# Kernel tuning notes

Hardware: AMD Instinct MI355X
Metric: run time of the kernel (lower is better)

Reference implementation:

```python
import jax, jax.numpy as jnp
import numpy as np
from jax import lax

D = 1024; L = 2; NS = 16; PD = 64; B_ = 64; K_ = 128; H_ = 32; W_ = 32


def setup_inputs():
    ks = jax.random.split(jax.random.key(0), 16)
    def rn(i, shape, s=0.02):
        return jax.random.normal(ks[i], shape, dtype=jnp.float32) * s
    return {
        "slots": jax.random.normal(ks[0], (B_, K_, D), dtype=jnp.float32),
        "keep_mask": jnp.ones((B_, K_), jnp.float32),
        "attn_maps": jax.random.uniform(ks[1], (B_, K_, H_ * W_), dtype=jnp.float32),
        "H": H_, "W": W_,
        "pos_W1": rn(2, (4 * PD, D)), "pos_b1": jnp.zeros((D,), jnp.float32),
        "pos_W2": rn(3, (D, D)), "pos_b2": jnp.zeros((D,), jnp.float32),
        "ssm_W_in": rn(4, (2, L, D, D)), "ssm_b_in": jnp.zeros((2, L, D), jnp.float32),
        "ssm_W_dt": rn(5, (2, L, D, D)), "ssm_b_dt": jnp.zeros((2, L, D), jnp.float32),
        "ssm_W_B": rn(6, (2, L, D, NS)), "ssm_W_C": rn(7, (2, L, D, NS)),
        "ssm_A_log": rn(8, (2, L, D, NS), 1.0), "ssm_D": rn(9, (2, L, D), 1.0),
        "ssm_W_out": rn(10, (2, L, D, D)), "ssm_b_out": jnp.zeros((2, L, D), jnp.float32),
        "merge_W": rn(11, (L, 2 * D, D)), "merge_b": jnp.zeros((L, D), jnp.float32),
        "norm_g": jnp.ones((L, D), jnp.float32), "norm_b": jnp.zeros((L, D), jnp.float32),
        "ffn_lng": jnp.ones((L, D), jnp.float32), "ffn_lnb": jnp.zeros((L, D), jnp.float32),
        "ffn_W1": rn(12, (L, D, 4 * D)), "ffn_b1": jnp.zeros((L, 4 * D), jnp.float32),
        "ffn_W2": rn(13, (L, 4 * D, D)), "ffn_b2": jnp.zeros((L, D), jnp.float32),
    }


def _ln(x, g, b):
    m = jnp.mean(x, -1, keepdims=True)
    v = jnp.mean((x - m) ** 2, -1, keepdims=True)
    return (x - m) * lax.rsqrt(v + 1e-5) * g + b


def _gelu(x):
    return jax.nn.gelu(x, approximate=False)


def _hilbert_order(centroids):
    # vectorized xy2d Hilbert index on a 16x16 grid, then argsort per batch
    gs = 16
    cx = jnp.clip(centroids[..., 0] * (gs - 1), 0, gs - 1).astype(jnp.int32)
    cy = jnp.clip(centroids[..., 1] * (gs - 1), 0, gs - 1).astype(jnp.int32)
    x, y = cx, cy
    d = jnp.zeros_like(cx)
    s = gs // 2
    while s > 0:
        rx = ((x & s) > 0).astype(jnp.int32)
        ry = ((y & s) > 0).astype(jnp.int32)
        d = d + s * s * ((3 * rx) ^ ry)
        x1 = jnp.where(rx == 1, s - 1 - x, x)
        y1 = jnp.where(rx == 1, s - 1 - y, y)
        xn = jnp.where(ry == 0, y1, x)
        yn = jnp.where(ry == 0, x1, y)
        x, y = xn, yn
        s //= 2
    return jnp.argsort(d, axis=-1)


def _ssm(x, W_in, b_in, W_dt, b_dt, W_B, W_C, A_log, D_skip, W_out, b_out):
    # Mamba-style diagonal selective scan: h_t = exp(dt*A)h_{t-1} + dt*B_t*u_t; y_t = C_t.h_t + D*u_t
    u = x @ W_in + b_in                    # [B,K,D]
    dt = jax.nn.softplus(x @ W_dt + b_dt)  # [B,K,D]
    Bc = x @ W_B                           # [B,K,NS]
    Cc = x @ W_C                           # [B,K,NS]
    A = -jnp.exp(A_log)                    # [D,NS]

    def step(h, inp):
        u_t, dt_t, B_t, C_t = inp
        h = jnp.exp(dt_t[..., None] * A) * h + dt_t[..., None] * B_t[:, None, :] * u_t[..., None]
        y = jnp.einsum('bdn,bn->bd', h, C_t) + D_skip * u_t
        return h, y

    h0 = jnp.zeros((x.shape[0], x.shape[-1], A.shape[-1]), x.dtype)
    xs = (u.swapaxes(0, 1), dt.swapaxes(0, 1), Bc.swapaxes(0, 1), Cc.swapaxes(0, 1))
    _, ys = lax.scan(step, h0, xs)
    return ys.swapaxes(0, 1) @ W_out + b_out


def _forward(slots, keep_mask, attn_maps, H, W, pos_W1, pos_b1, pos_W2, pos_b2,
             ssm_W_in, ssm_b_in, ssm_W_dt, ssm_b_dt, ssm_W_B, ssm_W_C, ssm_A_log,
             ssm_D, ssm_W_out, ssm_b_out, merge_W, merge_b, norm_g, norm_b,
             ffn_lng, ffn_lnb, ffn_W1, ffn_b1, ffn_W2, ffn_b2):
    B, K, Dm = slots.shape
    # slot centroids from attention maps
    attn = attn_maps[:, :K, :]
    gy = jnp.arange(H, dtype=slots.dtype) / max(H - 1, 1)
    gx = jnp.arange(W, dtype=slots.dtype) / max(W - 1, 1)
    grid_y, grid_x = jnp.meshgrid(gy, gx, indexing='ij')
    coords = jnp.stack([grid_x.ravel(), grid_y.ravel()], -1)  # [N,2]
    attn_prob = attn / (jnp.sum(attn, -1, keepdims=True) + 1e-8)
    centroids = jnp.einsum('bkn,nc->bkc', attn_prob, coords)  # [B,K,2]
    # sinusoidal spatial encoding of (centroid, spread)
    feats = jnp.concatenate([centroids, jnp.full_like(centroids, 0.1)], -1)  # [B,K,4]
    freqs = 1.0 / 10000.0 ** (jnp.arange(0, PD, 2, dtype=slots.dtype) / PD)
    ang = feats[..., None] * freqs * 3.14159                   # [B,K,4,PD/2]
    enc = jnp.concatenate([jnp.sin(ang), jnp.cos(ang)], -1).reshape(B, K, 4 * PD)
    pos_enc = _gelu(enc @ pos_W1 + pos_b1) @ pos_W2 + pos_b2
    slots = slots + pos_enc
    order = _hilbert_order(centroids)         # [B,K] (same every layer)
    reverse = jnp.argsort(order, -1)
    for i in range(merge_W.shape[0]):
        residual = slots
        ordered = jnp.take_along_axis(slots, order[..., None], 1)
        f = _ssm(ordered, ssm_W_in[0, i], ssm_b_in[0, i], ssm_W_dt[0, i], ssm_b_dt[0, i],
                 ssm_W_B[0, i], ssm_W_C[0, i], ssm_A_log[0, i], ssm_D[0, i],
                 ssm_W_out[0, i], ssm_b_out[0, i])
        bwd = jnp.flip(_ssm(jnp.flip(ordered, 1), ssm_W_in[1, i], ssm_b_in[1, i],
                            ssm_W_dt[1, i], ssm_b_dt[1, i], ssm_W_B[1, i], ssm_W_C[1, i],
                            ssm_A_log[1, i], ssm_D[1, i], ssm_W_out[1, i], ssm_b_out[1, i]), 1)
        merged = jnp.concatenate([f, bwd], -1) @ merge_W[i] + merge_b[i]
        unord = jnp.take_along_axis(merged, reverse[..., None], 1)
        slots = _ln(residual + unord, norm_g[i], norm_b[i])
        h = _ln(slots, ffn_lng[i], ffn_lnb[i])
        slots = slots + (_gelu(h @ ffn_W1[i] + ffn_b1[i]) @ ffn_W2[i] + ffn_b2[i])
        slots = slots * keep_mask[..., None]
    return slots, centroids


def reference(slots, keep_mask, attn_maps, H, W, pos_W1, pos_b1, pos_W2, pos_b2,
              ssm_W_in, ssm_b_in, ssm_W_dt, ssm_b_dt, ssm_W_B, ssm_W_C, ssm_A_log,
              ssm_D, ssm_W_out, ssm_b_out, merge_W, merge_b, norm_g, norm_b,
              ffn_lng, ffn_lnb, ffn_W1, ffn_b1, ffn_W2, ffn_b2):
    return _forward(slots, keep_mask, attn_maps, H, W, pos_W1, pos_b1, pos_W2, pos_b2,
                    ssm_W_in, ssm_b_in, ssm_W_dt, ssm_b_dt, ssm_W_B, ssm_W_C, ssm_A_log,
                    ssm_D, ssm_W_out, ssm_b_out, merge_W, merge_b, norm_g, norm_b,
                    ffn_lng, ffn_lnb, ffn_W1, ffn_b1, ffn_W2, ffn_b2)
```

## Files before the change

### kernel.cpp

```cpp
#include <hip/hip_runtime.h>
#include <hip/hip_bf16.h>
#include <math.h>

typedef __attribute__((ext_vector_type(8))) short short8;
typedef __attribute__((ext_vector_type(4))) float f32x4;
typedef __hip_bfloat16 bf16;

#define GAS(p) ((const __attribute__((address_space(1))) void*)(p))
#define LAS(p) ((__attribute__((address_space(3))) void*)(p))

__device__ __forceinline__ float gelu_exact(float x) {
    return 0.5f * x * (1.0f + erff(x * 0.70710678118654752f));
}
__device__ __forceinline__ float softplus_f(float x) {
    return (x > 20.f) ? x : log1pf(__expf(x));
}

__global__ void transpose_to_bf16(const float* __restrict__ in, bf16* __restrict__ out,
                                  int R, int C) {
    __shared__ float tile[32][33];
    int c0 = blockIdx.x * 32, r0 = blockIdx.y * 32;
    for (int i = threadIdx.y; i < 32; i += 8) {
        int r = r0 + i, c = c0 + threadIdx.x;
        tile[i][threadIdx.x] = (r < R && c < C) ? in[(size_t)r * C + c] : 0.f;
    }
    __syncthreads();
    for (int i = threadIdx.y; i < 32; i += 8) {
        int c = c0 + i, r = r0 + threadIdx.x;
        if (c < C && r < R) out[(size_t)c * R + r] = __float2bfloat16(tile[threadIdx.x][i]);
    }
}

__global__ void centroid_kernel(const float* __restrict__ attn, float* __restrict__ out_cent,
                                int* __restrict__ hd) {
    int row = blockIdx.x * 4 + (threadIdx.x >> 6);
    int lane = threadIdx.x & 63;
    const float* ap = attn + (size_t)row * 1024;
    float s = 0.f, sx = 0.f, sy = 0.f;
    for (int i = lane; i < 1024; i += 64) {
        float a = ap[i];
        float cxn = (float)(i & 31) * (1.0f / 31.0f);
        float cyn = (float)(i >> 5) * (1.0f / 31.0f);
        s += a; sx += a * cxn; sy += a * cyn;
    }
#pragma unroll
    for (int o = 32; o; o >>= 1) {
        s += __shfl_xor(s, o); sx += __shfl_xor(sx, o); sy += __shfl_xor(sy, o);
    }
    if (lane == 0) {
        float inv = 1.0f / (s + 1e-8f);
        float cx = sx * inv, cy = sy * inv;
        out_cent[row * 2] = cx;
        out_cent[row * 2 + 1] = cy;
        int x = (int)fminf(fmaxf(cx * 15.f, 0.f), 15.f);
        int y = (int)fminf(fmaxf(cy * 15.f, 0.f), 15.f);
        int d = 0;
        for (int s2 = 8; s2 > 0; s2 >>= 1) {
            int rx = (x & s2) ? 1 : 0, ry = (y & s2) ? 1 : 0;
            d += s2 * s2 * ((3 * rx) ^ ry);
            int x1 = rx ? (s2 - 1 - x) : x;
            int y1 = rx ? (s2 - 1 - y) : y;
            int xn = (ry == 0) ? y1 : x;
            int yn = (ry == 0) ? x1 : y;
            x = xn; y = yn;
        }
        hd[row] = d;
    }
}

__global__ void order_kernel(const int* __restrict__ hd, int* __restrict__ order) {
    __shared__ int dsh[128];
    int b = blockIdx.x, tid = threadIdx.x;
    dsh[tid] = hd[b * 128 + tid];
    __syncthreads();
    int mine = dsh[tid], rank = 0;
    for (int j = 0; j < 128; ++j) {
        int dj = dsh[j];
        rank += (dj < mine) || (dj == mine && j < tid);
    }
    order[b * 128 + rank] = tid;
}

__global__ void enc_kernel(const float* __restrict__ cent, bf16* __restrict__ enc) {
    int row = blockIdx.x, tid = threadIdx.x;
    int f = tid >> 6, s = tid & 63;
    float feat = (f == 0) ? cent[row * 2] : (f == 1) ? cent[row * 2 + 1] : 0.1f;
    int i = s & 31;
    float freq = powf(10000.f, -(float)i * (1.f / 32.f));
    float ang = feat * freq * 3.14159f;
    float v = (s < 32) ? sinf(ang) : cosf(ang);
    enc[(size_t)row * 256 + tid] = __float2bfloat16(v);
}

template <int EPI>
__launch_bounds__(256)
__global__ void gemm_bt(const bf16* __restrict__ A, int lda,
                        const bf16* __restrict__ Bt, int K, int ldc,
                        float* __restrict__ outF, bf16* __restrict__ outB,
                        const float* __restrict__ bias1, const float* __restrict__ bias2,
                        const float* __restrict__ resid, const float* __restrict__ mask) {
    __shared__ __align__(16) short a_sh[128 * 64];
    __shared__ __align__(16) short b_sh[128 * 64];
    const int tid = threadIdx.x;
    const int lane = tid & 63;
    const int wid = tid >> 6;
    const int wr = wid >> 1, wc = wid & 1;
    const int row0 = blockIdx.y * 128;
    const int col0 = blockIdx.x * 128;

    f32x4 acc[4][4] = {};

    const int nk = K >> 6;
    for (int kt = 0; kt < nk; ++kt) {
        __syncthreads();
#pragma unroll
        for (int c = 0; c < 4; ++c) {
            int slot = c * 256 + tid;
            int r = slot >> 3;
            int ks = (slot & 7) ^ (r & 7);
            const bf16* ga = A + (size_t)(row0 + r) * lda + (kt << 6) + (ks << 3);
            __builtin_amdgcn_global_load_lds(GAS(ga), LAS((char*)a_sh + slot * 16), 16, 0, 0);
            const bf16* gb = Bt + (size_t)(col0 + r) * K + (kt << 6) + (ks << 3);
            __builtin_amdgcn_global_load_lds(GAS(gb), LAS((char*)b_sh + slot * 16), 16, 0, 0);
        }
        __syncthreads();
#pragma unroll
        for (int kk = 0; kk < 2; ++kk) {
            short8 af[4], bfr[4];
            int kb = (kk << 2) + (lane >> 4);
#pragma unroll
            for (int m = 0; m < 4; ++m) {
                int r = wr * 64 + m * 16 + (lane & 15);
                af[m] = *(const short8*)(a_sh + ((r << 3) + (kb ^ (r & 7))) * 8);
            }
#pragma unroll
            for (int n = 0; n < 4; ++n) {
                int r = wc * 64 + n * 16 + (lane & 15);
                bfr[n] = *(const short8*)(b_sh + ((r << 3) + (kb ^ (r & 7))) * 8);
            }
#pragma unroll
            for (int m = 0; m < 4; ++m)
#pragma unroll
                for (int n = 0; n < 4; ++n)
                    acc[m][n] = __builtin_amdgcn_mfma_f32_16x16x32_bf16(af[m], bfr[n], acc[m][n], 0, 0, 0);
        }
    }

#pragma unroll
    for (int m = 0; m < 4; ++m) {
#pragma unroll
        for (int n = 0; n < 4; ++n) {
#pragma unroll
            for (int q = 0; q < 4; ++q) {
                int r = row0 + wr * 64 + m * 16 + ((lane >> 4) << 2) + q;
                int c = col0 + wc * 64 + n * 16 + (lane & 15);
                float v = acc[m][n][q];
                size_t idx = (size_t)r * ldc + c;
                if constexpr (EPI == 0) {
                    v = gelu_exact(v + bias1[c]);
                    outB[idx] = __float2bfloat16(v);
                } else if constexpr (EPI == 1) {
                    v += bias1[c] + resid[idx];
                    outF[idx] = v;
                    outB[idx] = __float2bfloat16(v);
                } else if constexpr (EPI == 2) {
                    if (c < 1024) {
                        outF[idx] = v + bias1[c];
                    } else if (c < 2048) {
                        outF[idx] = softplus_f(v + bias2[c - 1024]);
                    } else if (c < 2080) {
                        outF[idx] = v;
                    }
                } else if constexpr (EPI == 3) {
                    outB[idx] = __float2bfloat16(v + bias1[c]);
                } else if constexpr (EPI == 4) {
                    outF[idx] = v + bias1[c] + resid[(size_t)r * 1024 + c];
                } else {
                    float sv = resid[idx] + v + bias1[c];
                    sv *= mask[r];
                    outF[idx] = sv;
                    outB[idx] = __float2bfloat16(sv);
                }
            }
        }
    }
}

__launch_bounds__(256)
__global__ void scan_kernel(const float* __restrict__ udt, const int* __restrict__ order,
                            const float* __restrict__ A_log, const float* __restrict__ Dsk,
                            bf16* __restrict__ ycat, int layer, int dir) {
    __shared__ float bc_sh[128 * 32];
    __shared__ int ord_sh[128];
    const int tid = threadIdx.x;
    const int dch = blockIdx.x, b = blockIdx.y;
    if (tid < 128) ord_sh[tid] = order[b * 128 + tid];
    __syncthreads();
    for (int i = tid; i < 128 * 32; i += 256) {
        int t = i >> 5, n = i & 31;
        int p = ord_sh[t];
        bc_sh[i] = udt[(size_t)(b * 128 + p) * 2176 + 2048 + n];
    }
    __syncthreads();
    const int d = dch * 256 + tid;
    float a[16], h[16];
    const float* al = A_log + ((size_t)((dir * 2 + layer) * 1024 + d)) * 16;
#pragma unroll
    for (int n = 0; n < 16; ++n) { a[n] = -__expf(al[n]); h[n] = 0.f; }
    const float dsk = Dsk[(dir * 2 + layer) * 1024 + d];

    float uf[4], df[4];
#pragma unroll
    for (int j = 0; j < 4; ++j) {
        int t = dir ? (127 - j) : j;
        size_t rb = (size_t)(b * 128 + ord_sh[t]) * 2176;
        uf[j] = udt[rb + d];
        df[j] = udt[rb + 1024 + d];
    }
    for (int s0 = 0; s0 < 128; s0 += 4) {
#pragma unroll
        for (int j = 0; j < 4; ++j) {
            int s = s0 + j;
            int t = dir ? (127 - s) : s;
            float u = uf[j], dt = df[j];
            int s2 = s + 4;
            if (s2 < 128) {
                int t2 = dir ? (127 - s2) : s2;
                size_t rb2 = (size_t)(b * 128 + ord_sh[t2]) * 2176;
                uf[j] = udt[rb2 + d];
                df[j] = udt[rb2 + 1024 + d];
            }
            float y = dsk * u;
            float dtu = dt * u;
#pragma unroll
            for (int n = 0; n < 16; ++n) {
                h[n] = __expf(dt * a[n]) * h[n] + dtu * bc_sh[t * 32 + n];
                y += h[n] * bc_sh[t * 32 + 16 + n];
            }
            ycat[(size_t)(b * 128 + ord_sh[t]) * 2048 + dir * 1024 + d] = __float2bfloat16(y);
        }
    }
}

__launch_bounds__(256)
__global__ void ln2_kernel(const float* __restrict__ tmp, float* __restrict__ slots,
                           bf16* __restrict__ hout,
                           const float* __restrict__ g1, const float* __restrict__ b1,
                           const float* __restrict__ g2, const float* __restrict__ b2) {
    __shared__ float red[16];
    const int tid = threadIdx.x, row = blockIdx.x;
    const int lane = tid & 63, wid = tid >> 6;
    const float4 x = ((const float4*)(tmp + (size_t)row * 1024))[tid];
    float s = x.x + x.y + x.z + x.w;
    float ss = x.x * x.x + x.y * x.y + x.z * x.z + x.w * x.w;
#pragma unroll
    for (int o = 32; o; o >>= 1) { s += __shfl_xor(s, o); ss += __shfl_xor(ss, o); }
    if (lane == 0) { red[wid] = s; red[4 + wid] = ss; }
    __syncthreads();
    float S = red[0] + red[1] + red[2] + red[3];
    float SS = red[4] + red[5] + red[6] + red[7];
    float m = S * (1.f / 1024.f);
    float inv = rsqrtf(SS * (1.f / 1024.f) - m * m + 1e-5f);
    int c = tid * 4;
    float4 sv;
    sv.x = (x.x - m) * inv * g1[c] + b1[c];
    sv.y = (x.y - m) * inv * g1[c + 1] + b1[c + 1];
    sv.z = (x.z - m) * inv * g1[c + 2] + b1[c + 2];
    sv.w = (x.w - m) * inv * g1[c + 3] + b1[c + 3];
    ((float4*)(slots + (size_t)row * 1024))[tid] = sv;
    float s2 = sv.x + sv.y + sv.z + sv.w;
    float ss2 = sv.x * sv.x + sv.y * sv.y + sv.z * sv.z + sv.w * sv.w;
#pragma unroll
    for (int o = 32; o; o >>= 1) { s2 += __shfl_xor(s2, o); ss2 += __shfl_xor(ss2, o); }
    if (lane == 0) { red[8 + wid] = s2; red[12 + wid] = ss2; }
    __syncthreads();
    float S2 = red[8] + red[9] + red[10] + red[11];
    float SS2 = red[12] + red[13] + red[14] + red[15];
    float m2 = S2 * (1.f / 1024.f);
    float inv2 = rsqrtf(SS2 * (1.f / 1024.f) - m2 * m2 + 1e-5f);
    size_t ob = (size_t)row * 1024 + c;
    hout[ob]     = __float2bfloat16((sv.x - m2) * inv2 * g2[c] + b2[c]);
    hout[ob + 1] = __float2bfloat16((sv.y - m2) * inv2 * g2[c + 1] + b2[c + 1]);
    hout[ob + 2] = __float2bfloat16((sv.z - m2) * inv2 * g2[c + 2] + b2[c + 2]);
    hout[ob + 3] = __float2bfloat16((sv.w - m2) * inv2 * g2[c + 3] + b2[c + 3]);
}

static void launch_gemm(int epi, int N, hipStream_t st, const bf16* A, int lda,
                        const bf16* Bt, int K, int ldc, float* outF, bf16* outB,
                        const float* b1, const float* b2, const float* resid,
                        const float* mask) {
    dim3 grid(N / 128, 64);
    switch (epi) {
        case 0: gemm_bt<0><<<grid, 256, 0, st>>>(A, lda, Bt, K, ldc, outF, outB, b1, b2, resid, mask); break;
        case 1: gemm_bt<1><<<grid, 256, 0, st>>>(A, lda, Bt, K, ldc, outF, outB, b1, b2, resid, mask); break;
        case 2: gemm_bt<2><<<grid, 256, 0, st>>>(A, lda, Bt, K, ldc, outF, outB, b1, b2, resid, mask); break;
        case 3: gemm_bt<3><<<grid, 256, 0, st>>>(A, lda, Bt, K, ldc, outF, outB, b1, b2, resid, mask); break;
        case 4: gemm_bt<4><<<grid, 256, 0, st>>>(A, lda, Bt, K, ldc, outF, outB, b1, b2, resid, mask); break;
        default: gemm_bt<5><<<grid, 256, 0, st>>>(A, lda, Bt, K, ldc, outF, outB, b1, b2, resid, mask); break;
    }
}

static void launch_tr(hipStream_t st, const float* in, bf16* out, int R, int C) {
    dim3 g((C + 31) / 32, (R + 31) / 32);
    transpose_to_bf16<<<g, dim3(32, 8), 0, st>>>(in, out, R, C);
}

extern "C" void kernel_launch(void* const* d_in, const int* in_sizes, int n_in,
                              void* d_out, int out_size, void* d_ws, size_t ws_size,
                              hipStream_t stream) {
    (void)in_sizes; (void)n_in; (void)out_size;
    const float* slots_in = (const float*)d_in[0];
    const float* keep     = (const float*)d_in[1];
    const float* attn     = (const float*)d_in[2];
    const float* pos_W1   = (const float*)d_in[5];
    const float* pos_b1   = (const float*)d_in[6];
    const float* pos_W2   = (const float*)d_in[7];
    const float* pos_b2   = (const float*)d_in[8];
    const float* W_in     = (const float*)d_in[9];
    const float* b_in     = (const float*)d_in[10];
    const float* W_dt     = (const float*)d_in[11];
    const float* b_dt     = (const float*)d_in[12];
    const float* W_B      = (const float*)d_in[13];
    const float* W_C      = (const float*)d_in[14];
    const float* A_log    = (const float*)d_in[15];
    const float* Dsk      = (const float*)d_in[16];
    const float* W_out    = (const float*)d_in[17];
    const float* b_out    = (const float*)d_in[18];
    const float* merge_W  = (const float*)d_in[19];
    const float* merge_b  = (const float*)d_in[20];
    const float* norm_g   = (const float*)d_in[21];
    const float* norm_b   = (const float*)d_in[22];
    const float* ffn_lng  = (const float*)d_in[23];
    const float* ffn_lnb  = (const float*)d_in[24];
    const float* ffn_W1   = (const float*)d_in[25];
    const float* ffn_b1   = (const float*)d_in[26];
    const float* ffn_W2   = (const float*)d_in[27];
    const float* ffn_b2   = (const float*)d_in[28];

    float* out_slots = (float*)d_out;
    float* out_cent  = out_slots + (size_t)8192 * 1024;

    char* ws = (char*)d_ws;
    size_t off = 0;
    auto alloc = [&](size_t bytes) -> char* {
        char* r = ws + off;
        off += (bytes + 255) & ~(size_t)255;
        return r;
    };
    bf16* wpool    = (bf16*)alloc((size_t)4096 * 1024 * 2);
    bf16* slots_bf = (bf16*)alloc((size_t)8192 * 1024 * 2);
    int*  hd       = (int*)alloc((size_t)8192 * 4);
    int*  order    = (int*)alloc((size_t)8192 * 4);
    char* scratch  = alloc((size_t)104857600);
    if (ws_size < off) return;

    float* udt  = (float*)scratch;
    bf16*  ycat = (bf16*)(scratch + 71303168);
    bf16*  encb = (bf16*)scratch;
    bf16*  h1   = (bf16*)(scratch + 4194304);
    bf16*  fbwd = (bf16*)scratch;
    float* tmp  = (float*)(scratch + 33554432);
    bf16*  hbuf = (bf16*)(scratch + 71303168);
    bf16*  mid  = (bf16*)scratch;

    centroid_kernel<<<2048, 256, 0, stream>>>(attn, out_cent, hd);
    order_kernel<<<64, 128, 0, stream>>>(hd, order);
    enc_kernel<<<8192, 256, 0, stream>>>(out_cent, encb);

    bf16* posW1t = wpool;
    bf16* posW2t = wpool + 262144;
    launch_tr(stream, pos_W1, posW1t, 256, 1024);
    launch_tr(stream, pos_W2, posW2t, 1024, 1024);
    launch_gemm(0, 1024, stream, encb, 256, posW1t, 256, 1024, nullptr, h1,
                pos_b1, nullptr, nullptr, nullptr);
    launch_gemm(1, 1024, stream, h1, 1024, posW2t, 1024, 1024, out_slots, slots_bf,
                pos_b2, nullptr, slots_in, nullptr);

    for (int l = 0; l < 2; ++l) {
        for (int dir = 0; dir < 2; ++dir) {
            size_t wsl = (size_t)(dir * 2 + l);
            launch_tr(stream, W_in + wsl * 1048576, wpool, 1024, 1024);
            launch_tr(stream, W_dt + wsl * 1048576, wpool + (size_t)1024 * 1024, 1024, 1024);
            launch_tr(stream, W_B + wsl * 16384, wpool + (size_t)2048 * 1024, 1024, 16);
            launch_tr(stream, W_C + wsl * 16384, wpool + (size_t)2064 * 1024, 1024, 16);
            launch_gemm(2, 2176, stream, slots_bf, 1024, wpool, 1024, 2176, udt, nullptr,
                        b_in + wsl * 1024, b_dt + wsl * 1024, nullptr, nullptr);
            scan_kernel<<<dim3(4, 64), 256, 0, stream>>>(udt, order, A_log, Dsk, ycat, l, dir);
        }
        for (int dir = 0; dir < 2; ++dir) {
            size_t wsl = (size_t)(dir * 2 + l);
            launch_tr(stream, W_out + wsl * 1048576, wpool, 1024, 1024);
            launch_gemm(3, 1024, stream, ycat + dir * 1024, 2048, wpool, 1024, 2048,
                        nullptr, fbwd + dir * 1024, b_out + wsl * 1024, nullptr, nullptr, nullptr);
        }
        launch_tr(stream, merge_W + (size_t)l * 2097152, wpool, 2048, 1024);
        launch_gemm(4, 1024, stream, fbwd, 2048, wpool, 2048, 1024, tmp, nullptr,
                    merge_b + l * 1024, nullptr, out_slots, nullptr);
        ln2_kernel<<<8192, 256, 0, stream>>>(tmp, out_slots, hbuf,
                                             norm_g + l * 1024, norm_b + l * 1024,
                                             ffn_lng + l * 1024, ffn_lnb + l * 1024);
        launch_tr(stream, ffn_W1 + (size_t)l * 4194304, wpool, 1024, 4096);
        launch_gemm(0, 4096, stream, hbuf, 1024, wpool, 1024, 4096, nullptr, mid,
                    ffn_b1 + (size_t)l * 4096, nullptr, nullptr, nullptr);
        launch_tr(stream, ffn_W2 + (size_t)l * 4194304, wpool, 4096, 1024);
        launch_gemm(5, 1024, stream, mid, 4096, wpool, 4096, 1024, out_slots, slots_bf,
                    ffn_b2 + l * 1024, nullptr, out_slots, keep);
    }
}
```

Baseline: 1.919 ms.

## Use triple-buffered 128x256 GEMM tiles and split B/C projection into separate GEMM

Replaces the single-buffered 128x128 GEMM with a 512-thread 128x256 tile kernel that stages three K-slices ahead in LDS and uses explicit vmcnt waits, barriers and setprio. This overlaps global-to-LDS loads with MFMA work and raises the arithmetic intensity of each tile. The input projection is narrowed to 2048 columns so it fits the 256-wide tiling. The B/C projection (32 columns) now runs as a separate small GEMM into its own buffer, and the scan kernel reads from that buffer. Larger LDS use (about 144KB per block) and hand-written waitcnt logic add correctness risk and may lower occupancy.

```diff
diff --git a/kernel.cpp b/kernel.cpp
--- a/kernel.cpp
+++ b/kernel.cpp
@@ -93,57 +93,86 @@
 }
 
 template <int EPI>
-__launch_bounds__(256)
-__global__ void gemm_bt(const bf16* __restrict__ A, int lda,
-                        const bf16* __restrict__ Bt, int K, int ldc,
-                        float* __restrict__ outF, bf16* __restrict__ outB,
-                        const float* __restrict__ bias1, const float* __restrict__ bias2,
-                        const float* __restrict__ resid, const float* __restrict__ mask) {
-    __shared__ __align__(16) short a_sh[128 * 64];
-    __shared__ __align__(16) short b_sh[128 * 64];
+__launch_bounds__(512, 2)
+__global__ void gemm3(const bf16* __restrict__ A, int lda,
+                      const bf16* __restrict__ Bt, int K, int ldc,
+                      float* __restrict__ outF, bf16* __restrict__ outB,
+                      const float* __restrict__ bias1, const float* __restrict__ bias2,
+                      const float* __restrict__ resid, const float* __restrict__ mask) {
+    __shared__ __align__(16) short lds[3 * 24576];
     const int tid = threadIdx.x;
     const int lane = tid & 63;
     const int wid = tid >> 6;
-    const int wr = wid >> 1, wc = wid & 1;
+    const int wm = wid >> 2, wn = wid & 3;
     const int row0 = blockIdx.y * 128;
-    const int col0 = blockIdx.x * 128;
+    const int col0 = blockIdx.x * 256;
+
+    auto STAGE = [&](int kt, int b) {
+        short* base = lds + b * 24576;
+#pragma unroll
+        for (int l = 0; l < 2; ++l) {
+            int s = l * 512 + tid;
+            int r = s >> 3;
+            int ks = (s & 7) ^ (r & 7);
+            const bf16* ga = A + (size_t)(row0 + r) * lda + (kt << 6) + (ks << 3);
+            __builtin_amdgcn_global_load_lds(GAS(ga), LAS((char*)base + s * 16), 16, 0, 0);
+        }
+#pragma unroll
+        for (int l = 0; l < 4; ++l) {
+            int s = l * 512 + tid;
+            int r = s >> 3;
+            int ks = (s & 7) ^ (r & 7);
+            const bf16* gb = Bt + (size_t)(col0 + r) * K + (kt << 6) + (ks << 3);
+            __builtin_amdgcn_global_load_lds(GAS(gb), LAS((char*)base + 16384 + s * 16), 16, 0, 0);
+        }
+    };
 
     f32x4 acc[4][4] = {};
-
-    const int nk = K >> 6;
-    for (int kt = 0; kt < nk; ++kt) {
-        __syncthreads();
-#pragma unroll
-        for (int c = 0; c < 4; ++c) {
-            int slot = c * 256 + tid;
-            int r = slot >> 3;
-            int ks = (slot & 7) ^ (r & 7);
-            const bf16* ga = A + (size_t)(row0 + r) * lda + (kt << 6) + (ks << 3);
-            __builtin_amdgcn_global_load_lds(GAS(ga), LAS((char*)a_sh + slot * 16), 16, 0, 0);
-            const bf16* gb = Bt + (size_t)(col0 + r) * K + (kt << 6) + (ks << 3);
-            __builtin_amdgcn_global_load_lds(GAS(gb), LAS((char*)b_sh + slot * 16), 16, 0, 0);
-        }
-        __syncthreads();
+    const int nt = K >> 6;
+
+    STAGE(0, 0);
+    STAGE(1, 1);
+    STAGE(2, 2);
+    asm volatile("s_waitcnt vmcnt(12)" ::: "memory");
+    asm volatile("s_barrier" ::: "memory");
+
+    int cur = 0;
+    for (int t = 0; t < nt; ++t) {
+        short* abase = lds + cur * 24576;
+        short* bbase = abase + 8192;
+        short8 af[2][4], bfr[2][4];
 #pragma unroll
         for (int kk = 0; kk < 2; ++kk) {
-            short8 af[4], bfr[4];
             int kb = (kk << 2) + (lane >> 4);
 #pragma unroll
             for (int m = 0; m < 4; ++m) {
-                int r = wr * 64 + m * 16 + (lane & 15);
-                af[m] = *(const short8*)(a_sh + ((r << 3) + (kb ^ (r & 7))) * 8);
+                int r = wm * 64 + m * 16 + (lane & 15);
+                af[kk][m] = *(const short8*)(abase + ((r << 3) + (kb ^ (r & 7))) * 8);
             }
 #pragma unroll
             for (int n = 0; n < 4; ++n) {
-                int r = wc * 64 + n * 16 + (lane & 15);
-                bfr[n] = *(const short8*)(b_sh + ((r << 3) + (kb ^ (r & 7))) * 8);
-            }
+                int r = wn * 64 + n * 16 + (lane & 15);
+                bfr[kk][n] = *(const short8*)(bbase + ((r << 3) + (kb ^ (r & 7))) * 8);
+            }
+        }
+        asm volatile("s_waitcnt lgkmcnt(0)" ::: "memory");
+        asm volatile("s_barrier" ::: "memory");
+        if (t + 3 < nt) STAGE(t + 3, cur);
+        __builtin_amdgcn_s_setprio(1);
+#pragma unroll
+        for (int kk = 0; kk < 2; ++kk)
 #pragma unroll
             for (int m = 0; m < 4; ++m)
 #pragma unroll
                 for (int n = 0; n < 4; ++n)
-                    acc[m][n] = __builtin_amdgcn_mfma_f32_16x16x32_bf16(af[m], bfr[n], acc[m][n], 0, 0, 0);
-        }
+                    acc[m][n] = __builtin_amdgcn_mfma_f32_16x16x32_bf16(af[kk][m], bfr[kk][n], acc[m][n], 0, 0, 0);
+        __builtin_amdgcn_s_setprio(0);
+        int rem = nt - 2 - t;
+        if (rem >= 2)      { asm volatile("s_waitcnt vmcnt(12)" ::: "memory"); }
+        else if (rem == 1) { asm volatile("s_waitcnt vmcnt(6)"  ::: "memory"); }
+        else               { asm volatile("s_waitcnt vmcnt(0)"  ::: "memory"); }
+        asm volatile("s_barrier" ::: "memory");
+        cur = (cur == 2) ? 0 : cur + 1;
     }
 
 #pragma unroll
@@ -152,8 +181,8 @@
         for (int n = 0; n < 4; ++n) {
 #pragma unroll
             for (int q = 0; q < 4; ++q) {
-                int r = row0 + wr * 64 + m * 16 + ((lane >> 4) << 2) + q;
-                int c = col0 + wc * 64 + n * 16 + (lane & 15);
+                int r = row0 + wm * 64 + m * 16 + ((lane >> 4) << 2) + q;
+                int c = col0 + wn * 64 + n * 16 + (lane & 15);
                 float v = acc[m][n][q];
                 size_t idx = (size_t)r * ldc + c;
                 if constexpr (EPI == 0) {
@@ -164,13 +193,8 @@
                     outF[idx] = v;
                     outB[idx] = __float2bfloat16(v);
                 } else if constexpr (EPI == 2) {
-                    if (c < 1024) {
-                        outF[idx] = v + bias1[c];
-                    } else if (c < 2048) {
-                        outF[idx] = softplus_f(v + bias2[c - 1024]);
-                    } else if (c < 2080) {
-                        outF[idx] = v;
-                    }
+                    if (c < 1024) outF[idx] = v + bias1[c];
+                    else          outF[idx] = softplus_f(v + bias2[c - 1024]);
                 } else if constexpr (EPI == 3) {
                     outB[idx] = __float2bfloat16(v + bias1[c]);
                 } else if constexpr (EPI == 4) {
@@ -186,8 +210,78 @@
     }
 }
 
+template <int EPI>
 __launch_bounds__(256)
-__global__ void scan_kernel(const float* __restrict__ udt, const int* __restrict__ order,
+__global__ void gemm_bt(const bf16* __restrict__ A, int lda,
+                        const bf16* __restrict__ Bt, int K, int ldc,
+                        float* __restrict__ outF) {
+    __shared__ __align__(16) short a_sh[128 * 64];
+    __shared__ __align__(16) short b_sh[128 * 64];
+    const int tid = threadIdx.x;
+    const int lane = tid & 63;
+    const int wid = tid >> 6;
+    const int wr = wid >> 1, wc = wid & 1;
+    const int row0 = blockIdx.y * 128;
+    const int col0 = blockIdx.x * 128;
+
+    f32x4 acc[4][4] = {};
+
+    const int nk = K >> 6;
+    for (int kt = 0; kt < nk; ++kt) {
+        __syncthreads();
+#pragma unroll
+        for (int c = 0; c < 4; ++c) {
+            int slot = c * 256 + tid;
+            int r = slot >> 3;
+            int ks = (slot & 7) ^ (r & 7);
+            const bf16* ga = A + (size_t)(row0 + r) * lda + (kt << 6) + (ks << 3);
+            __builtin_amdgcn_global_load_lds(GAS(ga), LAS((char*)a_sh + slot * 16), 16, 0, 0);
+            const bf16* gb = Bt + (size_t)(col0 + r) * K + (kt << 6) + (ks << 3);
+            __builtin_amdgcn_global_load_lds(GAS(gb), LAS((char*)b_sh + slot * 16), 16, 0, 0);
+        }
+        __syncthreads();
+#pragma unroll
+        for (int kk = 0; kk < 2; ++kk) {
+            short8 af[4], bfr[4];
+            int kb = (kk << 2) + (lane >> 4);
+#pragma unroll
+            for (int m = 0; m < 4; ++m) {
+                int r = wr * 64 + m * 16 + (lane & 15);
+                af[m] = *(const short8*)(a_sh + ((r << 3) + (kb ^ (r & 7))) * 8);
+            }
+#pragma unroll
+            for (int n = 0; n < 4; ++n) {
+                int r = wc * 64 + n * 16 + (lane & 15);
+                bfr[n] = *(const short8*)(b_sh + ((r << 3) + (kb ^ (r & 7))) * 8);
+            }
+#pragma unroll
+            for (int m = 0; m < 4; ++m)
+#pragma unroll
+                for (int n = 0; n < 4; ++n)
+                    acc[m][n] = __builtin_amdgcn_mfma_f32_16x16x32_bf16(af[m], bfr[n], acc[m][n], 0, 0, 0);
+        }
+    }
+
+#pragma unroll
+    for (int m = 0; m < 4; ++m) {
+#pragma unroll
+        for (int n = 0; n < 4; ++n) {
+#pragma unroll
+            for (int q = 0; q < 4; ++q) {
+                int r = row0 + wr * 64 + m * 16 + ((lane >> 4) << 2) + q;
+                int c = col0 + wc * 64 + n * 16 + (lane & 15);
+                float v = acc[m][n][q];
+                if constexpr (EPI == 6) {
+                    if (c < 32) outF[(size_t)r * 32 + c] = v;
+                }
+            }
+        }
+    }
+}
+
+__launch_bounds__(256)
+__global__ void scan_kernel(const float* __restrict__ udt, const float* __restrict__ bc,
+                            const int* __restrict__ order,
                             const float* __restrict__ A_log, const float* __restrict__ Dsk,
                             bf16* __restrict__ ycat, int layer, int dir) {
     __shared__ float bc_sh[128 * 32];
@@ -199,7 +293,7 @@
     for (int i = tid; i < 128 * 32; i += 256) {
         int t = i >> 5, n = i & 31;
         int p = ord_sh[t];
-        bc_sh[i] = udt[(size_t)(b * 128 + p) * 2176 + 2048 + n];
+        bc_sh[i] = bc[(size_t)(b * 128 + p) * 32 + n];
     }
     __syncthreads();
     const int d = dch * 256 + tid;
@@ -213,7 +307,7 @@
 #pragma unroll
     for (int j = 0; j < 4; ++j) {
         int t = dir ? (127 - j) : j;
-        size_t rb = (size_t)(b * 128 + ord_sh[t]) * 2176;
+        size_t rb = (size_t)(b * 128 + ord_sh[t]) * 2048;
         uf[j] = udt[rb + d];
         df[j] = udt[rb + 1024 + d];
     }
@@ -226,7 +320,7 @@
             int s2 = s + 4;
             if (s2 < 128) {
                 int t2 = dir ? (127 - s2) : s2;
-                size_t rb2 = (size_t)(b * 128 + ord_sh[t2]) * 2176;
+                size_t rb2 = (size_t)(b * 128 + ord_sh[t2]) * 2048;
                 uf[j] = udt[rb2 + d];
                 df[j] = udt[rb2 + 1024 + d];
             }
@@ -285,18 +379,18 @@
     hout[ob + 3] = __float2bfloat16((sv.w - m2) * inv2 * g2[c + 3] + b2[c + 3]);
 }
 
-static void launch_gemm(int epi, int N, hipStream_t st, const bf16* A, int lda,
-                        const bf16* Bt, int K, int ldc, float* outF, bf16* outB,
-                        const float* b1, const float* b2, const float* resid,
-                        const float* mask) {
-    dim3 grid(N / 128, 64);
+static void launch_gemm3(int epi, int N, hipStream_t st, const bf16* A, int lda,
+                         const bf16* Bt, int K, int ldc, float* outF, bf16* outB,
+                         const float* b1, const float* b2, const float* resid,
+                         const float* mask) {
+    dim3 grid(N / 256, 64);
     switch (epi) {
-        case 0: gemm_bt<0><<<grid, 256, 0, st>>>(A, lda, Bt, K, ldc, outF, outB, b1, b2, resid, mask); break;
-        case 1: gemm_bt<1><<<grid, 256, 0, st>>>(A, lda, Bt, K, ldc, outF, outB, b1, b2, resid, mask); break;
-        case 2: gemm_bt<2><<<grid, 256, 0, st>>>(A, lda, Bt, K, ldc, outF, outB, b1, b2, resid, mask); break;
-        case 3: gemm_bt<3><<<grid, 256, 0, st>>>(A, lda, Bt, K, ldc, outF, outB, b1, b2, resid, mask); break;
-        case 4: gemm_bt<4><<<grid, 256, 0, st>>>(A, lda, Bt, K, ldc, outF, outB, b1, b2, resid, mask); break;
-        default: gemm_bt<5><<<grid, 256, 0, st>>>(A, lda, Bt, K, ldc, outF, outB, b1, b2, resid, mask); break;
+        case 0: gemm3<0><<<grid, 512, 0, st>>>(A, lda, Bt, K, ldc, outF, outB, b1, b2, resid, mask); break;
+        case 1: gemm3<1><<<grid, 512, 0, st>>>(A, lda, Bt, K, ldc, outF, outB, b1, b2, resid, mask); break;
+        case 2: gemm3<2><<<grid, 512, 0, st>>>(A, lda, Bt, K, ldc, outF, outB, b1, b2, resid, mask); break;
+        case 3: gemm3<3><<<grid, 512, 0, st>>>(A, lda, Bt, K, ldc, outF, outB, b1, b2, resid, mask); break;
+        case 4: gemm3<4><<<grid, 512, 0, st>>>(A, lda, Bt, K, ldc, outF, outB, b1, b2, resid, mask); break;
+        default: gemm3<5><<<grid, 512, 0, st>>>(A, lda, Bt, K, ldc, outF, outB, b1, b2, resid, mask); break;
     }
 }
 
@@ -351,16 +445,17 @@
     bf16* slots_bf = (bf16*)alloc((size_t)8192 * 1024 * 2);
     int*  hd       = (int*)alloc((size_t)8192 * 4);
     int*  order    = (int*)alloc((size_t)8192 * 4);
-    char* scratch  = alloc((size_t)104857600);
+    char* scratch  = alloc((size_t)102760448);
     if (ws_size < off) return;
 
     float* udt  = (float*)scratch;
-    bf16*  ycat = (bf16*)(scratch + 71303168);
+    float* bcb  = (float*)(scratch + 67108864);
+    bf16*  ycat = (bf16*)(scratch + 68157440);
     bf16*  encb = (bf16*)scratch;
     bf16*  h1   = (bf16*)(scratch + 4194304);
     bf16*  fbwd = (bf16*)scratch;
     float* tmp  = (float*)(scratch + 33554432);
-    bf16*  hbuf = (bf16*)(scratch + 71303168);
+    bf16*  hbuf = (bf16*)(scratch + 68157440);
     bf16*  mid  = (bf16*)scratch;
 
     centroid_kernel<<<2048, 256, 0, stream>>>(attn, out_cent, hd);
@@ -371,10 +466,10 @@
     bf16* posW2t = wpool + 262144;
     launch_tr(stream, pos_W1, posW1t, 256, 1024);
     launch_tr(stream, pos_W2, posW2t, 1024, 1024);
-    launch_gemm(0, 1024, stream, encb, 256, posW1t, 256, 1024, nullptr, h1,
-                pos_b1, nullptr, nullptr, nullptr);
-    launch_gemm(1, 1024, stream, h1, 1024, posW2t, 1024, 1024, out_slots, slots_bf,
-                pos_b2, nullptr, slots_in, nullptr);
+    launch_gemm3(0, 1024, stream, encb, 256, posW1t, 256, 1024, nullptr, h1,
+                 pos_b1, nullptr, nullptr, nullptr);
+    launch_gemm3(1, 1024, stream, h1, 1024, posW2t, 1024, 1024, out_slots, slots_bf,
+                 pos_b2, nullptr, slots_in, nullptr);
 
     for (int l = 0; l < 2; ++l) {
         for (int dir = 0; dir < 2; ++dir) {
@@ -383,27 +478,29 @@
             launch_tr(stream, W_dt + wsl * 1048576, wpool + (size_t)1024 * 1024, 1024, 1024);
             launch_tr(stream, W_B + wsl * 16384, wpool + (size_t)2048 * 1024, 1024, 16);
             launch_tr(stream, W_C + wsl * 16384, wpool + (size_t)2064 * 1024, 1024, 16);
-            launch_gemm(2, 2176, stream, slots_bf, 1024, wpool, 1024, 2176, udt, nullptr,
-                        b_in + wsl * 1024, b_dt + wsl * 1024, nullptr, nullptr);
-            scan_kernel<<<dim3(4, 64), 256, 0, stream>>>(udt, order, A_log, Dsk, ycat, l, dir);
+            launch_gemm3(2, 2048, stream, slots_bf, 1024, wpool, 1024, 2048, udt, nullptr,
+                         b_in + wsl * 1024, b_dt + wsl * 1024, nullptr, nullptr);
+            gemm_bt<6><<<dim3(1, 64), 256, 0, stream>>>(slots_bf, 1024,
+                         wpool + (size_t)2048 * 1024, 1024, 32, bcb);
+            scan_kernel<<<dim3(4, 64), 256, 0, stream>>>(udt, bcb, order, A_log, Dsk, ycat, l, dir);
         }
         for (int dir = 0; dir < 2; ++dir) {
             size_t wsl = (size_t)(dir * 2 + l);
             launch_tr(stream, W_out + wsl * 1048576, wpool, 1024, 1024);
-            launch_gemm(3, 1024, stream, ycat + dir * 1024, 2048, wpool, 1024, 2048,
-                        nullptr, fbwd + dir * 1024, b_out + wsl * 1024, nullptr, nullptr, nullptr);
+            launch_gemm3(3, 1024, stream, ycat + dir * 1024, 2048, wpool, 1024, 2048,
+                         nullptr, fbwd + dir * 1024, b_out + wsl * 1024, nullptr, nullptr, nullptr);
         }
         launch_tr(stream, merge_W + (size_t)l * 2097152, wpool, 2048, 1024);
-        launch_gemm(4, 1024, stream, fbwd, 2048, wpool, 2048, 1024, tmp, nullptr,
-                    merge_b + l * 1024, nullptr, out_slots, nullptr);
+        launch_gemm3(4, 1024, stream, fbwd, 2048, wpool, 2048, 1024, tmp, nullptr,
+                     merge_b + l * 1024, nullptr, out_slots, nullptr);
         ln2_kernel<<<8192, 256, 0, stream>>>(tmp, out_slots, hbuf,
                                              norm_g + l * 1024, norm_b + l * 1024,
                                              ffn_lng + l * 1024, ffn_lnb + l * 1024);
         launch_tr(stream, ffn_W1 + (size_t)l * 4194304, wpool, 1024, 4096);
-        launch_gemm(0, 4096, stream, hbuf, 1024, wpool, 1024, 4096, nullptr, mid,
-                    ffn_b1 + (size_t)l * 4096, nullptr, nullptr, nullptr);
+        launch_gemm3(0, 4096, stream, hbuf, 1024, wpool, 1024, 4096, nullptr, mid,
+                     ffn_b1 + (size_t)l * 4096, nullptr, nullptr, nullptr);
         launch_tr(stream, ffn_W2 + (size_t)l * 4194304, wpool, 4096, 1024);
-        launch_gemm(5, 1024, stream, mid, 4096, wpool, 4096, 1024, out_slots, slots_bf,
-                    ffn_b2 + l * 1024, nullptr, out_slots, keep);
-    }
-}
+        launch_gemm3(5, 1024, stream, mid, 4096, wpool, 4096, 1024, out_slots, slots_bf,
+                     ffn_b2 + l * 1024, nullptr, out_slots, keep);
+    }
+}
```

Measured after the change: 1.991 ms. 3.7% more time.
